# Kernel optimization log

Hardware: AMD Instinct MI355X
Metric: run time of the kernel (lower is better)

The kernel has to match this reference:

```python
import jax, jax.numpy as jnp
import numpy as np

B, N = 2, 256
RC = 6.0
BOX = 12.0
# (center_radius, eta) for G2; kappas for G3; (eta, zeta, lambda) for G4/G5
G2_PARAMS = [(rs, eta) for rs in (0.0, 2.0) for eta in (0.1, 1.0)]
G3_KAPPAS = [1.0, 2.0]
G45_PARAMS = [(eta, zeta, lam) for eta in (0.01, 0.1) for zeta in (1.0, 4.0) for lam in (-1.0, 1.0)]


def _fc(r, rc):
    # Behler cosine cutoff: 0.5*(cos(pi r / rc) + 1) for r < rc, else 0
    return 0.5 * (jnp.cos(jnp.pi * r / rc) + 1.0) * (r < rc)


def setup_inputs() -> dict:
    key = jax.random.key(0)
    k1, k2 = jax.random.split(key)
    atomic_numbers = jax.random.randint(k1, (N,), 1, 10).astype(jnp.float32)
    coordinates = jax.random.uniform(k2, (B, N, 3), dtype=jnp.float32) * BOX
    return {"atomic_numbers": atomic_numbers, "coordinates": coordinates}


def reference(atomic_numbers, coordinates):
    b, n, _ = coordinates.shape
    # r_ij vector = x_i - x_j, matching coords.unsqueeze(-2) - coords.unsqueeze(-3)
    dvec = coordinates[:, :, None, :] - coordinates[:, None, :, :]        # [B,N,N,3]
    sq = jnp.sum(dvec * dvec, axis=-1)                                    # [B,N,N]
    pair_mask = ~jnp.eye(n, dtype=bool)                                   # j != i
    sq_safe = jnp.where(pair_mask, sq, 1.0)
    r = jnp.where(pair_mask, jnp.sqrt(sq_safe), 0.0)                      # [B,N,N]
    fcr = _fc(r, RC) * pair_mask                                          # cutoff, self excluded

    feats = [jnp.broadcast_to(atomic_numbers, (b, n))]
    # G1: sum_j fc(r_ij)
    feats.append(jnp.sum(fcr, axis=-1))
    # G2: sum_j exp(-eta*(r_ij - Rs)^2) * fc(r_ij)
    for rs, eta in G2_PARAMS:
        feats.append(jnp.sum(jnp.exp(-eta * (r - rs) ** 2) * fcr, axis=-1))
    # G3: sum_j cos(kappa * r_ij) * fc(r_ij)
    for kappa in G3_KAPPAS:
        feats.append(jnp.sum(jnp.cos(kappa * r) * fcr, axis=-1))

    # shared angular (triplet) quantities, each [B,N,N,N]
    dot = jnp.einsum('bijc,bikc->bijk', dvec, dvec)
    denom = r[:, :, :, None] * r[:, :, None, :]
    cos_t = dot / jnp.where(denom > 0, denom, 1.0)
    sq_ij = sq[:, :, :, None]
    sq_ik = sq[:, :, None, :]
    sq_jk = sq[:, None, :, :]
    sq3 = sq_ij + sq_ik + sq_jk
    sq2 = sq_ij + sq_ik
    # fc products: fcr already zero on the diagonal, so fc3 vanishes whenever
    # j==i, k==i, or j==k (full triplet mask for G4)
    fc3 = fcr[:, :, :, None] * fcr[:, :, None, :] * fcr[:, None, :, :]
    fc2 = fcr[:, :, :, None] * fcr[:, :, None, :] * pair_mask[None, None, :, :]

    # G4: 2^(1-zeta) sum_{j!=k} (1+lam*cos)^zeta exp(-eta*(rij^2+rik^2+rjk^2)) fc fc fc
    for eta, zeta, lam in G45_PARAMS:
        ang = jnp.maximum(1.0 + lam * cos_t, 0.0) ** zeta
        feats.append((2.0 ** (1.0 - zeta)) * jnp.sum(ang * jnp.exp(-eta * sq3) * fc3, axis=(-2, -1)))
    # G5: 2^(1-zeta) sum_{j!=k} (1+lam*cos)^zeta exp(-eta*(rij^2+rik^2)) fc fc
    for eta, zeta, lam in G45_PARAMS:
        ang = jnp.maximum(1.0 + lam * cos_t, 0.0) ** zeta
        feats.append((2.0 ** (1.0 - zeta)) * jnp.sum(ang * jnp.exp(-eta * sq2) * fc2, axis=(-2, -1)))

    return jnp.stack(feats, axis=-1)  # [B, N, 24]
```

## Files before the change

kernel.cpp:

```cpp
#include <hip/hip_runtime.h>
#include <math.h>

#define NN 256
#define NF 24
#define RCUT 6.0f
#define PI_F 3.14159265358979323846f
#define CS 0.27415568f

__device__ __forceinline__ float fc_poly(float u) {
    float p = 1.0438378e-9f;
    p = fmaf(p, u, -1.3778659e-7f);
    p = fmaf(p, u,  1.2400794e-5f);
    p = fmaf(p, u, -6.9444444e-4f);
    p = fmaf(p, u,  2.0833333e-2f);
    p = fmaf(p, u, -0.25f);
    p = fmaf(p, u,  1.0f);
    return p;
}

__global__ __launch_bounds__(512, 4) void feat_kernel(
    const float* __restrict__ Z,
    const float* __restrict__ coords,
    float* __restrict__ out)
{
    const int i = blockIdx.x, b = blockIdx.y;
    const int tid = threadIdx.x, lane = tid & 63, wave = tid >> 6;

    __shared__ float4 geo[NN + 128];
    __shared__ float4 ab[NN + 128];
    __shared__ int   wave_cnt[4];
    __shared__ float rad[4][7];
    __shared__ float red[6][8][8];
    __shared__ float mom[2][64][36];
    __shared__ float momsum[2][36];

    const float* cb = coords + (size_t)b * NN * 3;
    const float xi = cb[i * 3 + 0], yi = cb[i * 3 + 1], zi = cb[i * 3 + 2];

    float dx = 0, dy = 0, dz = 0, r2 = 0, r = 0, fc = 0;
    bool incut = false;
    if (tid < NN) {
        const float xj = cb[tid * 3 + 0], yj = cb[tid * 3 + 1], zj = cb[tid * 3 + 2];
        dx = xi - xj; dy = yi - yj; dz = zi - zj;
        r2 = dx * dx + dy * dy + dz * dz;
        r  = sqrtf(r2);
        incut = (tid != i) && (r < RCUT);
        fc = incut ? 0.5f * (__cosf((PI_F / RCUT) * r) + 1.0f) : 0.0f;
        float racc[7];
        racc[0] = fc;
        racc[1] = __expf(-0.1f * r2) * fc;
        racc[2] = __expf(-1.0f * r2) * fc;
        const float d = r - 2.0f;
        racc[3] = __expf(-0.1f * d * d) * fc;
        racc[4] = __expf(-1.0f * d * d) * fc;
        racc[5] = __cosf(r) * fc;
        racc[6] = __cosf(2.0f * r) * fc;
#pragma unroll
        for (int t = 0; t < 7; t++) {
            float v = racc[t];
            for (int off = 32; off > 0; off >>= 1) v += __shfl_down(v, off, 64);
            if (lane == 0) rad[wave][t] = v;
        }
        const unsigned long long bal = __ballot(incut);
        if (lane == 0) wave_cnt[wave] = __popcll(bal);
    }
    __syncthreads();

    const int m = wave_cnt[0] + wave_cnt[1] + wave_cnt[2] + wave_cnt[3];
    if (tid < NN && incut) {
        const unsigned long long bal = __ballot(incut);
        int base = 0;
#pragma unroll
        for (int w = 0; w < 4; w++) if (w < wave) base += wave_cnt[w];
        const int p = base + __popcll(bal & ((1ULL << lane) - 1ULL));
        const float rinv = 1.0f / r;
        geo[p] = make_float4(dx * rinv, dy * rinv, dz * rinv, r);
        ab[p]  = make_float4(fc * __expf(-0.01f * r2), fc * __expf(-0.1f * r2), r2, 0.0f);
    }
    __syncthreads();
    const int Rext = (m >= 2) ? ((m - 1) >> 1) : 0;
    for (int s = tid; s < Rext; s += 512) { geo[m + s] = geo[s]; ab[m + s] = ab[s]; }
    __syncthreads();

    if (wave < 6) {
        float acc[8];
#pragma unroll
        for (int t = 0; t < 8; t++) acc[t] = 0.0f;
        if (m >= 2) {
            const int Rfull = (m - 1) >> 1;
            const int tlo = 1 + (Rfull * wave) / 6;
            const int thi = (Rfull * (wave + 1)) / 6;
            const int mh = m >> 1;
            const bool doHalf = (wave == 5) && ((m & 1) == 0);
            for (int rnd = 0; rnd < 4; ++rnd) {
                const int jj = lane + (rnd << 6);
                if (jj >= m) break;
                const float4 gj = geo[jj];
                const float4 aj = ab[jj];
                const float r2j = aj.z;
                const float gw2 = -2.0f * gj.w;
                const int tend = thi + ((doHalf && jj < mh) ? 1 : 0);
                for (int t = tlo; t <= tend; ++t) {
                    const int kk = jj + ((t > thi) ? mh : t);
                    const float4 g = geo[kk];
                    const float4 a = ab[kk];
                    const float cost = fmaf(gj.x, g.x, fmaf(gj.y, g.y, gj.z * g.z));
                    const float s = fmaf(gw2 * g.w, cost, r2j + a.z);
                    const float pfc = fc_poly(CS * s);
                    const float fcjk = (s < 36.0f) ? pfc : 0.0f;
                    const float ea = __expf(-0.01f * s);
                    const float eb = __expf(-0.1f * s);
                    const float wa = (aj.x * a.x) * (fcjk * ea);
                    const float wb = (aj.y * a.y) * (fcjk * eb);
                    const float c1m = 1.0f - cost, c1p = 1.0f + cost;
                    const float c2m = c1m * c1m, c2p = c1p * c1p;
                    const float c4m = c2m * c2m, c4p = c2p * c2p;
                    acc[0] += c1m * wa;  acc[1] += c1p * wa;
                    acc[2] += c4m * wa;  acc[3] += c4p * wa;
                    acc[4] += c1m * wb;  acc[5] += c1p * wb;
                    acc[6] += c4m * wb;  acc[7] += c4p * wb;
                }
            }
        }
#pragma unroll
        for (int t = 0; t < 8; t++) {
            float v = acc[t];
            v += __shfl_down(v, 32, 64);
            v += __shfl_down(v, 16, 64);
            v += __shfl_down(v, 8, 64);
            acc[t] = v;
        }
        if (lane < 8) {
#pragma unroll
            for (int t = 0; t < 8; t++) red[wave][lane][t] = acc[t];
        }
    } else {
        const int e = wave - 6;
        float mm[36];
#pragma unroll
        for (int q = 0; q < 36; q++) mm[q] = 0.0f;
        for (int rnd = 0; rnd < 4; ++rnd) {
            const int jj = lane + (rnd << 6);
            if (jj >= m) break;
            const float4 g = geo[jj];
            const float4 a = ab[jj];
            const float w = (e == 0) ? a.x : a.y;
            const float x = g.x, y = g.y, z = g.z;
            mm[0] += w;
            const float wx = w * x, wy = w * y, wz = w * z;
            mm[1] += wx; mm[2] += wy; mm[3] += wz;
            const float wxx = wx * x, wxy = wx * y, wxz = wx * z;
            const float wyy = wy * y, wyz = wy * z, wzz = wz * z;
            mm[4] += wxx; mm[5] += wxy; mm[6] += wxz;
            mm[7] += wyy; mm[8] += wyz; mm[9] += wzz;
            const float wxxx = wxx * x, wxxy = wxx * y, wxxz = wxx * z;
            const float wxyy = wxy * y, wxyz = wxy * z, wxzz = wxz * z;
            const float wyyy = wyy * y, wyyz = wyy * z, wyzz = wyz * z, wzzz = wzz * z;
            mm[10] += wxxx; mm[11] += wxxy; mm[12] += wxxz; mm[13] += wxyy;
            mm[14] += wxyz; mm[15] += wxzz; mm[16] += wyyy; mm[17] += wyyz;
            mm[18] += wyzz; mm[19] += wzzz;
            mm[20] += wxxx * x; mm[21] += wxxx * y; mm[22] += wxxx * z;
            mm[23] += wxxy * y; mm[24] += wxxy * z; mm[25] += wxxz * z;
            mm[26] += wxyy * y; mm[27] += wxyy * z; mm[28] += wxyz * z;
            mm[29] += wxzz * z; mm[30] += wyyy * y; mm[31] += wyyy * z;
            mm[32] += wyyz * z; mm[33] += wyzz * z; mm[34] += wzzz * z;
            mm[35] = fmaf(w, w, mm[35]);
        }
#pragma unroll
        for (int q = 0; q < 36; q++) mom[e][lane][q] = mm[q];
        if (lane < 36) {
            float v0 = 0, v1 = 0, v2 = 0, v3 = 0;
#pragma unroll
            for (int j = 0; j < 64; j += 4) {
                v0 += mom[e][j + 0][lane]; v1 += mom[e][j + 1][lane];
                v2 += mom[e][j + 2][lane]; v3 += mom[e][j + 3][lane];
            }
            momsum[e][lane] = (v0 + v1) + (v2 + v3);
        }
    }
    __syncthreads();

    float* ob = out + ((size_t)b * NN + i) * NF;
    if (tid < 64) {
        const int f = tid >> 3, s = tid & 7;
        float v = 0.0f;
#pragma unroll
        for (int w = 0; w < 6; w++) v += red[w][s][f];
        v += __shfl_down(v, 4, 8);
        v += __shfl_down(v, 2, 8);
        v += __shfl_down(v, 1, 8);
        if (s == 0) {
            v *= ((f & 3) >= 2) ? 0.25f : 2.0f;
            ob[8 + f] = v;
        }
    } else if (tid < 72) {
        const int f = tid - 64, e = f >> 2, sub = f & 3;
        const float* M = momsum[e];
        const float S0 = M[0] * M[0];
        const float S1 = M[1] * M[1] + M[2] * M[2] + M[3] * M[3];
        const float S2 = M[4] * M[4] + M[7] * M[7] + M[9] * M[9]
                       + 2.f * (M[5] * M[5] + M[6] * M[6] + M[8] * M[8]);
        const float S3 = M[10] * M[10] + M[16] * M[16] + M[19] * M[19]
                       + 3.f * (M[11] * M[11] + M[12] * M[12] + M[13] * M[13]
                              + M[15] * M[15] + M[17] * M[17] + M[18] * M[18])
                       + 6.f * M[14] * M[14];
        const float S4 = M[20] * M[20] + M[30] * M[30] + M[34] * M[34]
                       + 4.f * (M[21] * M[21] + M[22] * M[22] + M[26] * M[26]
                              + M[29] * M[29] + M[31] * M[31] + M[33] * M[33])
                       + 6.f * (M[23] * M[23] + M[25] * M[25] + M[32] * M[32])
                       + 12.f * (M[24] * M[24] + M[27] * M[27] + M[28] * M[28]);
        const float D = M[35];
        const float lam = (sub & 1) ? 1.0f : -1.0f;
        float v;
        if (sub < 2) v = S0 + lam * S1 - (1.0f + lam) * D;
        else         v = 0.125f * (S0 + 6.f * S2 + S4 + lam * 4.f * (S1 + S3)
                                   - ((sub == 3) ? 16.f * D : 0.0f));
        ob[16 + f] = v;
    } else if (tid < 79) {
        const int t = tid - 72;
        ob[1 + t] = rad[0][t] + rad[1][t] + rad[2][t] + rad[3][t];
    } else if (tid == 79) {
        ob[0] = Z[i];
    }
}

extern "C" void kernel_launch(void* const* d_in, const int* in_sizes, int n_in,
                              void* d_out, int out_size, void* d_ws, size_t ws_size,
                              hipStream_t stream) {
    const float* Z = (const float*)d_in[0];
    const float* coords = (const float*)d_in[1];
    float* out = (float*)d_out;
    feat_kernel<<<dim3(NN, 2), dim3(512), 0, stream>>>(Z, coords, out);
}
```

Baseline: 63.81 us.

## Split the two eta values across a grid z-dimension to double block count

Adds a third grid dimension that picks the eta value, so each block computes only one eta's G4 triplet terms and G5 moments. All 8 waves now do triplet work and wave 0 computes the moments in the same block. This halves the per-block exponential and accumulator work and doubles the number of blocks to raise GPU occupancy. The cost is that neighbour compaction and the geometry setup now run twice per atom, and wave 0 carries extra moment work serially.

```diff
diff --git a/kernel.cpp b/kernel.cpp
--- a/kernel.cpp
+++ b/kernel.cpp
@@ -23,16 +23,17 @@
     const float* __restrict__ coords,
     float* __restrict__ out)
 {
-    const int i = blockIdx.x, b = blockIdx.y;
+    const int i = blockIdx.x, b = blockIdx.y, e = blockIdx.z;
     const int tid = threadIdx.x, lane = tid & 63, wave = tid >> 6;
+    const float ETA = e ? 0.1f : 0.01f;
 
     __shared__ float4 geo[NN + 128];
-    __shared__ float4 ab[NN + 128];
+    __shared__ float2 ab[NN + 128];
     __shared__ int   wave_cnt[4];
     __shared__ float rad[4][7];
-    __shared__ float red[6][8][8];
-    __shared__ float mom[2][64][36];
-    __shared__ float momsum[2][36];
+    __shared__ float red[8][8][4];
+    __shared__ float mom[64][36];
+    __shared__ float momsum[36];
 
     const float* cb = coords + (size_t)b * NN * 3;
     const float xi = cb[i * 3 + 0], yi = cb[i * 3 + 1], zi = cb[i * 3 + 2];
@@ -46,20 +47,22 @@
         r  = sqrtf(r2);
         incut = (tid != i) && (r < RCUT);
         fc = incut ? 0.5f * (__cosf((PI_F / RCUT) * r) + 1.0f) : 0.0f;
-        float racc[7];
-        racc[0] = fc;
-        racc[1] = __expf(-0.1f * r2) * fc;
-        racc[2] = __expf(-1.0f * r2) * fc;
-        const float d = r - 2.0f;
-        racc[3] = __expf(-0.1f * d * d) * fc;
-        racc[4] = __expf(-1.0f * d * d) * fc;
-        racc[5] = __cosf(r) * fc;
-        racc[6] = __cosf(2.0f * r) * fc;
-#pragma unroll
-        for (int t = 0; t < 7; t++) {
-            float v = racc[t];
-            for (int off = 32; off > 0; off >>= 1) v += __shfl_down(v, off, 64);
-            if (lane == 0) rad[wave][t] = v;
+        if (e == 0) {
+            float racc[7];
+            racc[0] = fc;
+            racc[1] = __expf(-0.1f * r2) * fc;
+            racc[2] = __expf(-1.0f * r2) * fc;
+            const float d = r - 2.0f;
+            racc[3] = __expf(-0.1f * d * d) * fc;
+            racc[4] = __expf(-1.0f * d * d) * fc;
+            racc[5] = __cosf(r) * fc;
+            racc[6] = __cosf(2.0f * r) * fc;
+#pragma unroll
+            for (int t = 0; t < 7; t++) {
+                float v = racc[t];
+                for (int off = 32; off > 0; off >>= 1) v += __shfl_down(v, off, 64);
+                if (lane == 0) rad[wave][t] = v;
+            }
         }
         const unsigned long long bal = __ballot(incut);
         if (lane == 0) wave_cnt[wave] = __popcll(bal);
@@ -75,67 +78,58 @@
         const int p = base + __popcll(bal & ((1ULL << lane) - 1ULL));
         const float rinv = 1.0f / r;
         geo[p] = make_float4(dx * rinv, dy * rinv, dz * rinv, r);
-        ab[p]  = make_float4(fc * __expf(-0.01f * r2), fc * __expf(-0.1f * r2), r2, 0.0f);
+        ab[p]  = make_float2(fc * __expf(-ETA * r2), r2);
     }
     __syncthreads();
     const int Rext = (m >= 2) ? ((m - 1) >> 1) : 0;
     for (int s = tid; s < Rext; s += 512) { geo[m + s] = geo[s]; ab[m + s] = ab[s]; }
     __syncthreads();
 
-    if (wave < 6) {
-        float acc[8];
-#pragma unroll
-        for (int t = 0; t < 8; t++) acc[t] = 0.0f;
-        if (m >= 2) {
-            const int Rfull = (m - 1) >> 1;
-            const int tlo = 1 + (Rfull * wave) / 6;
-            const int thi = (Rfull * (wave + 1)) / 6;
-            const int mh = m >> 1;
-            const bool doHalf = (wave == 5) && ((m & 1) == 0);
-            for (int rnd = 0; rnd < 4; ++rnd) {
-                const int jj = lane + (rnd << 6);
-                if (jj >= m) break;
-                const float4 gj = geo[jj];
-                const float4 aj = ab[jj];
-                const float r2j = aj.z;
-                const float gw2 = -2.0f * gj.w;
-                const int tend = thi + ((doHalf && jj < mh) ? 1 : 0);
-                for (int t = tlo; t <= tend; ++t) {
-                    const int kk = jj + ((t > thi) ? mh : t);
-                    const float4 g = geo[kk];
-                    const float4 a = ab[kk];
-                    const float cost = fmaf(gj.x, g.x, fmaf(gj.y, g.y, gj.z * g.z));
-                    const float s = fmaf(gw2 * g.w, cost, r2j + a.z);
-                    const float pfc = fc_poly(CS * s);
-                    const float fcjk = (s < 36.0f) ? pfc : 0.0f;
-                    const float ea = __expf(-0.01f * s);
-                    const float eb = __expf(-0.1f * s);
-                    const float wa = (aj.x * a.x) * (fcjk * ea);
-                    const float wb = (aj.y * a.y) * (fcjk * eb);
-                    const float c1m = 1.0f - cost, c1p = 1.0f + cost;
-                    const float c2m = c1m * c1m, c2p = c1p * c1p;
-                    const float c4m = c2m * c2m, c4p = c2p * c2p;
-                    acc[0] += c1m * wa;  acc[1] += c1p * wa;
-                    acc[2] += c4m * wa;  acc[3] += c4p * wa;
-                    acc[4] += c1m * wb;  acc[5] += c1p * wb;
-                    acc[6] += c4m * wb;  acc[7] += c4p * wb;
-                }
+    float acc[4] = {0.0f, 0.0f, 0.0f, 0.0f};
+    if (m >= 2) {
+        const int Rfull = (m - 1) >> 1;
+        const int tlo = 1 + ((Rfull * wave) >> 3);
+        const int thi = (Rfull * (wave + 1)) >> 3;
+        const int mh = m >> 1;
+        const bool doHalf = (wave == 7) && ((m & 1) == 0);
+        for (int rnd = 0; rnd < 4; ++rnd) {
+            const int jj = lane + (rnd << 6);
+            if (jj >= m) break;
+            const float4 gj = geo[jj];
+            const float2 aj = ab[jj];
+            const float r2j = aj.y;
+            const float gw2 = -2.0f * gj.w;
+            const int tend = thi + ((doHalf && jj < mh) ? 1 : 0);
+            for (int t = tlo; t <= tend; ++t) {
+                const int kk = jj + ((t > thi) ? mh : t);
+                const float4 g = geo[kk];
+                const float2 a = ab[kk];
+                const float cost = fmaf(gj.x, g.x, fmaf(gj.y, g.y, gj.z * g.z));
+                const float s = fmaf(gw2 * g.w, cost, r2j + a.y);
+                const float pfc = fc_poly(CS * s);
+                const float fcjk = (s < 36.0f) ? pfc : 0.0f;
+                const float w3 = (aj.x * a.x) * (fcjk * __expf(-ETA * s));
+                const float c1m = 1.0f - cost, c1p = 1.0f + cost;
+                const float c2m = c1m * c1m, c2p = c1p * c1p;
+                acc[0] += c1m * w3;          acc[1] += c1p * w3;
+                acc[2] += c2m * c2m * w3;    acc[3] += c2p * c2p * w3;
             }
         }
-#pragma unroll
-        for (int t = 0; t < 8; t++) {
-            float v = acc[t];
-            v += __shfl_down(v, 32, 64);
-            v += __shfl_down(v, 16, 64);
-            v += __shfl_down(v, 8, 64);
-            acc[t] = v;
-        }
-        if (lane < 8) {
-#pragma unroll
-            for (int t = 0; t < 8; t++) red[wave][lane][t] = acc[t];
-        }
-    } else {
-        const int e = wave - 6;
+    }
+#pragma unroll
+    for (int t = 0; t < 4; t++) {
+        float v = acc[t];
+        v += __shfl_down(v, 32, 64);
+        v += __shfl_down(v, 16, 64);
+        v += __shfl_down(v, 8, 64);
+        acc[t] = v;
+    }
+    if (lane < 8) {
+#pragma unroll
+        for (int t = 0; t < 4; t++) red[wave][lane][t] = acc[t];
+    }
+
+    if (wave == 0) {
         float mm[36];
 #pragma unroll
         for (int q = 0; q < 36; q++) mm[q] = 0.0f;
@@ -143,8 +137,7 @@
             const int jj = lane + (rnd << 6);
             if (jj >= m) break;
             const float4 g = geo[jj];
-            const float4 a = ab[jj];
-            const float w = (e == 0) ? a.x : a.y;
+            const float w = ab[jj].x;
             const float x = g.x, y = g.y, z = g.z;
             mm[0] += w;
             const float wx = w * x, wy = w * y, wz = w * z;
@@ -167,35 +160,35 @@
             mm[35] = fmaf(w, w, mm[35]);
         }
 #pragma unroll
-        for (int q = 0; q < 36; q++) mom[e][lane][q] = mm[q];
+        for (int q = 0; q < 36; q++) mom[lane][q] = mm[q];
         if (lane < 36) {
             float v0 = 0, v1 = 0, v2 = 0, v3 = 0;
 #pragma unroll
             for (int j = 0; j < 64; j += 4) {
-                v0 += mom[e][j + 0][lane]; v1 += mom[e][j + 1][lane];
-                v2 += mom[e][j + 2][lane]; v3 += mom[e][j + 3][lane];
+                v0 += mom[j + 0][lane]; v1 += mom[j + 1][lane];
+                v2 += mom[j + 2][lane]; v3 += mom[j + 3][lane];
             }
-            momsum[e][lane] = (v0 + v1) + (v2 + v3);
+            momsum[lane] = (v0 + v1) + (v2 + v3);
         }
     }
     __syncthreads();
 
     float* ob = out + ((size_t)b * NN + i) * NF;
-    if (tid < 64) {
+    if (tid < 32) {
         const int f = tid >> 3, s = tid & 7;
         float v = 0.0f;
 #pragma unroll
-        for (int w = 0; w < 6; w++) v += red[w][s][f];
+        for (int w = 0; w < 8; w++) v += red[w][s][f];
         v += __shfl_down(v, 4, 8);
         v += __shfl_down(v, 2, 8);
         v += __shfl_down(v, 1, 8);
         if (s == 0) {
-            v *= ((f & 3) >= 2) ? 0.25f : 2.0f;
-            ob[8 + f] = v;
-        }
-    } else if (tid < 72) {
-        const int f = tid - 64, e = f >> 2, sub = f & 3;
-        const float* M = momsum[e];
+            v *= (f >= 2) ? 0.25f : 2.0f;
+            ob[8 + 4 * e + f] = v;
+        }
+    } else if (tid < 36) {
+        const int sub = tid - 32;
+        const float* M = momsum;
         const float S0 = M[0] * M[0];
         const float S1 = M[1] * M[1] + M[2] * M[2] + M[3] * M[3];
         const float S2 = M[4] * M[4] + M[7] * M[7] + M[9] * M[9]
@@ -215,11 +208,11 @@
         if (sub < 2) v = S0 + lam * S1 - (1.0f + lam) * D;
         else         v = 0.125f * (S0 + 6.f * S2 + S4 + lam * 4.f * (S1 + S3)
                                    - ((sub == 3) ? 16.f * D : 0.0f));
-        ob[16 + f] = v;
-    } else if (tid < 79) {
-        const int t = tid - 72;
+        ob[16 + 4 * e + sub] = v;
+    } else if (e == 0 && tid >= 36 && tid < 43) {
+        const int t = tid - 36;
         ob[1 + t] = rad[0][t] + rad[1][t] + rad[2][t] + rad[3][t];
-    } else if (tid == 79) {
+    } else if (e == 0 && tid == 43) {
         ob[0] = Z[i];
     }
 }
@@ -230,5 +223,5 @@
     const float* Z = (const float*)d_in[0];
     const float* coords = (const float*)d_in[1];
     float* out = (float*)d_out;
-    feat_kernel<<<dim3(NN, 2), dim3(512), 0, stream>>>(Z, coords, out);
+    feat_kernel<<<dim3(NN, 2, 2), dim3(512), 0, stream>>>(Z, coords, out);
 }
```

After: 63.09 us. No clear change (-1.1%).
